# Kernel optimization log

Hardware: AMD Instinct MI355X
Metric: run time of the kernel (lower is better)

The kernel has to match this reference:

```python
import jax, jax.numpy as jnp
import numpy as np

VEC, HID, B, S = 1280, 128, 4, 256
EPS = 1e-5


def _ln(x):
    m = x.mean(-1, keepdims=True)
    v = ((x - m) ** 2).mean(-1, keepdims=True)
    return (x - m) / jnp.sqrt(v + EPS)


def _add_attn(q_in, kv_in, Wq, Wk, wv):
    # Additive (Bahdanau) attention: scores[b,i,j] = wv . tanh(q[b,i] + k[b,j])
    q = q_in @ Wq            # [B, Sq, H]
    k = kv_in @ Wk           # [B, Sk, H]
    feat = jnp.tanh(q[:, :, None, :] + k[:, None, :, :])   # [B, Sq, Sk, H]
    scores = jnp.einsum('bijh,h->bij', feat, wv)
    attn = jax.nn.softmax(scores, axis=-1)
    return jnp.einsum('bij,bjd->bid', attn, kv_in)          # values = kv_in


def _res_fc(x, W1, b1, W2, b2):
    return jnp.maximum(x @ W1 + b1, 0.0) @ W2 + b2 + x


def setup_inputs() -> dict:
    key = jax.random.key(0)
    ks = iter(jax.random.split(key, 64))
    d = {
        'X': jax.random.normal(next(ks), (B, S, VEC), dtype=jnp.float32),
        'lys_pos': 100,
    }
    sc = 0.02
    for i in (1, 2, 3, 4):
        d[f'Wq{i}'] = jax.random.normal(next(ks), (VEC, HID), dtype=jnp.float32) * sc
        d[f'Wk{i}'] = jax.random.normal(next(ks), (VEC, HID), dtype=jnp.float32) * sc
        d[f'wv{i}'] = jax.random.normal(next(ks), (HID,), dtype=jnp.float32) * sc
    for i in (1, 2, 3):
        d[f'rW1_{i}'] = jax.random.normal(next(ks), (VEC, HID), dtype=jnp.float32) * sc
        d[f'rb1_{i}'] = jnp.zeros((HID,), dtype=jnp.float32)
        d[f'rW2_{i}'] = jax.random.normal(next(ks), (HID, VEC), dtype=jnp.float32) * sc
        d[f'rb2_{i}'] = jnp.zeros((VEC,), dtype=jnp.float32)
    d['hW1'] = jax.random.normal(next(ks), (VEC, 32), dtype=jnp.float32) * sc
    d['hb1'] = jnp.zeros((32,), dtype=jnp.float32)
    d['hW2'] = jax.random.normal(next(ks), (32, 12), dtype=jnp.float32) * sc
    d['hb2'] = jnp.zeros((12,), dtype=jnp.float32)
    d['hW3'] = jax.random.normal(next(ks), (12, 2), dtype=jnp.float32) * sc
    d['hb3'] = jnp.zeros((2,), dtype=jnp.float32)
    return d


def reference(X, lys_pos,
              Wq1, Wk1, wv1, Wq2, Wk2, wv2, Wq3, Wk3, wv3, Wq4, Wk4, wv4,
              rW1_1, rb1_1, rW2_1, rb2_1,
              rW1_2, rb1_2, rW2_2, rb2_2,
              rW1_3, rb1_3, rW2_3, rb2_3,
              hW1, hb1, hW2, hb2, hW3, hb3):
    X = X.astype(jnp.float32)
    X = _ln(_add_attn(X, X, Wq1, Wk1, wv1) + X)
    X = _res_fc(X, rW1_1, rb1_1, rW2_1, rb2_1)
    X = _ln(_add_attn(X, X, Wq2, Wk2, wv2) + X)
    X = _res_fc(X, rW1_2, rb1_2, rW2_2, rb2_2)
    X = _ln(_add_attn(X, X, Wq3, Wk3, wv3) + X)
    X = _res_fc(X, rW1_3, rb1_3, rW2_3, rb2_3)
    X_lys = X[:, lys_pos, :][:, None, :]                    # [B, 1, VEC]
    X_lys = _ln(_add_attn(X_lys, X, Wq4, Wk4, wv4) + X_lys)
    h = jnp.maximum(X_lys @ hW1 + hb1, 0.0)                 # dropout = identity (eval)
    h = jnp.maximum(h @ hW2 + hb2, 0.0)
    logits = (h @ hW3 + hb3)[:, 0, :]                       # squeeze(1) -> [B, 2]
    return logits
```

## Files before the change

kernel.cpp:

```cpp
#include <hip/hip_runtime.h>


#define DEV __device__ __forceinline__

static constexpr int VEC = 1280;
static constexpr int HID = 128;
static constexpr int BB  = 4;
static constexpr int SS  = 256;
static constexpr int NPART = 8;
static constexpr long QK_PS = 262144;
static constexpr long H_PS  = 131072;
static constexpr int NBLK  = 512;
static constexpr int NSPLIT_NONE = 1 << 30;

typedef float f32x4 __attribute__((ext_vector_type(4)));

struct Params {
  const float* X; const int* lys;
  const float* Wq[4]; const float* Wk[4]; const float* wv[4];
  const float* rW1[3]; const float* rb1[3]; const float* rW2[3]; const float* rb2[3];
  const float* hW1; const float* hb1; const float* hW2; const float* hb2;
  const float* hW3; const float* hb3;
  float* QKp[4]; float* Qd[4]; float* KT[4];
  float* attn[3]; float* Yraw[3]; float* Yb[3];
  float* Hp[3]; float* Xout[3];
  float* out;
  unsigned* bar;
};

DEV void stcc(float* p, float v) {
  union { float f; unsigned u; } c; c.f = v;
  __hip_atomic_store((unsigned*)p, c.u, __ATOMIC_RELAXED,
                     __HIP_MEMORY_SCOPE_AGENT);
}
DEV void stcc4(float* p, float x, float y, float z, float w) {
  f32x4 v; v[0] = x; v[1] = y; v[2] = z; v[3] = w;
  asm volatile("global_store_dwordx4 %0, %1, off sc0 sc1"
               :: "v"(p), "v"(v) : "memory");
}

DEV float ftanh(float x) {
  float e = __expf(2.0f * x);
  return 1.0f - __fdividef(2.0f, e + 1.0f);
}

DEV float waveSum(float v) {
#pragma unroll
  for (int off = 32; off > 0; off >>= 1) v += __shfl_xor(v, off, 64);
  return v;
}
DEV float waveMax(float v) {
#pragma unroll
  for (int off = 32; off > 0; off >>= 1) v = fmaxf(v, __shfl_xor(v, off, 64));
  return v;
}
DEV float blockSum(float v, float* red) {
  v = waveSum(v);
  int tid = threadIdx.x;
  if ((tid & 63) == 0) red[tid >> 6] = v;
  __syncthreads();
  float r = (red[0] + red[1]) + (red[2] + red[3]);
  __syncthreads();
  return r;
}
DEV float blockMax(float v, float* red) {
  v = waveMax(v);
  int tid = threadIdx.x;
  if ((tid & 63) == 0) red[tid >> 6] = v;
  __syncthreads();
  float r = fmaxf(fmaxf(red[0], red[1]), fmaxf(red[2], red[3]));
  __syncthreads();
  return r;
}

DEV void gsync(unsigned* bar, unsigned target) {
  __syncthreads();
  if (threadIdx.x == 0) {
    asm volatile("s_waitcnt vmcnt(0)" ::: "memory");
    unsigned* grp  = bar + ((blockIdx.x >> 6) << 5);
    unsigned* root = bar + 256;
    unsigned* gen  = bar + 288;
    unsigned c = __hip_atomic_fetch_add(grp, 1u, __ATOMIC_RELAXED,
                                        __HIP_MEMORY_SCOPE_AGENT);
    if (c + 1u == target * 64u) {
      unsigned r = __hip_atomic_fetch_add(root, 1u, __ATOMIC_RELAXED,
                                          __HIP_MEMORY_SCOPE_AGENT);
      if (r + 1u == target * 8u) {
        __hip_atomic_store(gen, target, __ATOMIC_RELAXED,
                           __HIP_MEMORY_SCOPE_AGENT);
      }
    }
    while (__hip_atomic_load(gen, __ATOMIC_RELAXED,
                             __HIP_MEMORY_SCOPE_AGENT) < target)
      __builtin_amdgcn_s_sleep(2);
  }
  __syncthreads();
}

template <int MODE, bool AFUSE, bool OBIAS, bool ORES>
DEV void gemm_task(int n0, int m0, int z,
                   const float* __restrict__ A, long sAb, long aPart,
                   const float* __restrict__ B0, const float* __restrict__ B1,
                   int nSplitB, long sBb, int ldB,
                   float* __restrict__ C, long sCb,
                   const float* __restrict__ aBias,
                   const float* __restrict__ oBias,
                   const float* __restrict__ res,
                   int N, int K, int kChunk) {
  __shared__ float As[16][68];
  __shared__ float Bs[16][68];

  const float* Ab = A + (MODE == 2 ? (long)z * sAb : 0L);
  float*       Cb = C + (MODE >= 1 ? (long)z * sCb : 0L);
  const float* resz = ORES ? (res + (MODE == 2 ? (long)z * sCb : 0L)) : nullptr;
  const float* Bsel;
  int nb;
  if (n0 < nSplitB) { Bsel = B0; nb = n0; } else { Bsel = B1; nb = n0 - nSplitB; }
  if (MODE == 2) Bsel += (long)z * sBb;

  const int kBeg = (MODE == 1) ? z * kChunk : 0;
  const int kEnd = (MODE == 1) ? kBeg + kChunk : K;

  const int tid = threadIdx.x;
  const int tx = tid & 15, ty = tid >> 4;
  const int ar = tid >> 2, ac = (tid & 3) << 2;
  const int br = tid >> 4, bc = (tid & 15) << 2;

  auto loadA = [&](int kt) -> float4 {
    const size_t aoff = (size_t)(m0 + ar) * K + kt + ac;
    if (AFUSE) {
      float4 s = *(const float4*)(Ab + aoff);
#pragma unroll
      for (int p = 1; p < NPART; ++p) {
        const float4 t = *(const float4*)(Ab + (long)p * aPart + aoff);
        s.x += t.x; s.y += t.y; s.z += t.z; s.w += t.w;
      }
      const float4 bz = *(const float4*)(aBias + kt + ac);
      s.x = fmaxf(s.x + bz.x, 0.0f);
      s.y = fmaxf(s.y + bz.y, 0.0f);
      s.z = fmaxf(s.z + bz.z, 0.0f);
      s.w = fmaxf(s.w + bz.w, 0.0f);
      return s;
    }
    return *(const float4*)(Ab + aoff);
  };
  auto loadB = [&](int kt) -> float4 {
    return *(const float4*)(Bsel + (size_t)(kt + br) * ldB + nb + bc);
  };
  auto stAB = [&](const float4& a4, const float4& b4) {
    As[ac + 0][ar] = a4.x;
    As[ac + 1][ar] = a4.y;
    As[ac + 2][ar] = a4.z;
    As[ac + 3][ar] = a4.w;
    *(float4*)&Bs[br][bc] = b4;
  };

  float acc[4][4] = {};
  auto domath = [&]() {
#pragma unroll
    for (int kk = 0; kk < 16; ++kk) {
      const float4 av = *(const float4*)&As[kk][ty << 2];
      const float4 bv = *(const float4*)&Bs[kk][tx << 2];
      const float a[4] = {av.x, av.y, av.z, av.w};
      const float b[4] = {bv.x, bv.y, bv.z, bv.w};
#pragma unroll
      for (int i = 0; i < 4; ++i)
#pragma unroll
        for (int j = 0; j < 4; ++j) acc[i][j] = fmaf(a[i], b[j], acc[i][j]);
    }
  };

  if constexpr (!AFUSE) {
    float4 aA = loadA(kBeg), bA = loadB(kBeg);
    float4 aB = aA, bB = bA;
    if (kBeg + 16 < kEnd) { aB = loadA(kBeg + 16); bB = loadB(kBeg + 16); }
    for (int kt = kBeg; kt < kEnd; kt += 32) {
      __syncthreads();
      stAB(aA, bA);
      __syncthreads();
      if (kt + 32 < kEnd) { aA = loadA(kt + 32); bA = loadB(kt + 32); }
      domath();
      if (kt + 16 < kEnd) {
        __syncthreads();
        stAB(aB, bB);
        __syncthreads();
        if (kt + 48 < kEnd) { aB = loadA(kt + 48); bB = loadB(kt + 48); }
        domath();
      }
    }
  } else {
    float4 a4 = loadA(kBeg), b4 = loadB(kBeg);
    for (int kt = kBeg; kt < kEnd; kt += 16) {
      __syncthreads();
      stAB(a4, b4);
      __syncthreads();
      if (kt + 16 < kEnd) { a4 = loadA(kt + 16); b4 = loadB(kt + 16); }
      domath();
    }
  }

#pragma unroll
  for (int i = 0; i < 4; ++i) {
    const int m = m0 + (ty << 2) + i;
    const int n = n0 + (tx << 2);
    float o[4] = {acc[i][0], acc[i][1], acc[i][2], acc[i][3]};
    if (OBIAS) {
#pragma unroll
      for (int j = 0; j < 4; ++j) o[j] += oBias[n + j];
    }
    if (ORES) {
      const float4 r4 = *(const float4*)(resz + (size_t)m * N + n);
      o[0] += r4.x; o[1] += r4.y; o[2] += r4.z; o[3] += r4.w;
    }
    stcc4(&Cb[(size_t)m * N + n], o[0], o[1], o[2], o[3]);
  }
}

DEV void qksum_task(int r, const float* __restrict__ QKp,
                    float* __restrict__ Qd, float* __restrict__ KT) {
  const int tid = threadIdx.x;
  const int b = r >> 8, j = r & 255;
  const size_t off = (size_t)r * 256 + tid;
  float v = 0.0f;
#pragma unroll
  for (int p = 0; p < NPART; ++p) v += QKp[(long)p * QK_PS + off];
  if (tid < 128) {
    stcc(Qd + (size_t)r * 128 + tid, v);
  } else {
    stcc(KT + (size_t)b * 32768 + (size_t)(tid - 128) * 256 + j, v);
  }
}

DEV void scores_task(int t, const float* __restrict__ Qd,
                     const float* __restrict__ KT,
                     const float* __restrict__ wv,
                     float* __restrict__ attn) {
  const int b = t >> 7, i0 = (t & 127) << 1, tid = threadIdx.x;
  __shared__ float qs[2][128], wvs[128], red[4];
  {
    const int rr = tid >> 7, h = tid & 127;
    qs[rr][h] = Qd[(size_t)(b * 256 + i0 + rr) * 128 + h];
  }
  if (tid < 128) wvs[tid] = wv[tid];
  __syncthreads();

  const float* KTb = KT + (size_t)b * 32768 + tid;
  float s0 = 0.0f, s1 = 0.0f;
#pragma unroll 4
  for (int h = 0; h < 128; h += 4) {
    const float k0 = KTb[(h + 0) * 256];
    const float k1 = KTb[(h + 1) * 256];
    const float k2 = KTb[(h + 2) * 256];
    const float k3 = KTb[(h + 3) * 256];
    const float w0 = wvs[h], w1 = wvs[h + 1], w2 = wvs[h + 2], w3 = wvs[h + 3];
    s0 += w0 * ftanh(qs[0][h] + k0) + w1 * ftanh(qs[0][h + 1] + k1) +
          w2 * ftanh(qs[0][h + 2] + k2) + w3 * ftanh(qs[0][h + 3] + k3);
    s1 += w0 * ftanh(qs[1][h] + k0) + w1 * ftanh(qs[1][h + 1] + k1) +
          w2 * ftanh(qs[1][h + 2] + k2) + w3 * ftanh(qs[1][h + 3] + k3);
  }
  {
    const float mx = blockMax(s0, red);
    const float e = __expf(s0 - mx);
    const float tot = blockSum(e, red);
    stcc(attn + (size_t)(b * 256 + i0) * 256 + tid, e / tot);
  }
  {
    const float mx = blockMax(s1, red);
    const float e = __expf(s1 - mx);
    const float tot = blockSum(e, red);
    stcc(attn + (size_t)(b * 256 + i0 + 1) * 256 + tid, e / tot);
  }
}

DEV void ln_task(int r, const float* __restrict__ A, float* __restrict__ Y) {
  __shared__ float red[4];
  __shared__ float xbuf[1280];
  const int tid = threadIdx.x;
  const float* a = A + (size_t)r * VEC;
  float v[5];
  float sum = 0.0f;
#pragma unroll
  for (int k = 0; k < 5; ++k) {
    v[k] = a[tid + k * 256];
    sum += v[k];
  }
  sum = blockSum(sum, red);
  const float m = sum * (1.0f / VEC);
  float sq = 0.0f;
#pragma unroll
  for (int k = 0; k < 5; ++k) {
    const float dl = v[k] - m;
    sq += dl * dl;
  }
  sq = blockSum(sq, red);
  const float rstd = rsqrtf(sq * (1.0f / VEC) + 1e-5f);
#pragma unroll
  for (int k = 0; k < 5; ++k) xbuf[tid + k * 256] = (v[k] - m) * rstd;
  __syncthreads();
  float* y = Y + (size_t)r * VEC;
  {
    const float* x = xbuf + (tid << 2);
    stcc4(y + (tid << 2), x[0], x[1], x[2], x[3]);
  }
  if (tid < 64) {
    const float* x = xbuf + 1024 + (tid << 2);
    stcc4(y + 1024 + (tid << 2), x[0], x[1], x[2], x[3]);
  }
  __syncthreads();
}

DEV void tail_task(int b, const Params& p) {
  __shared__ float qs[128], wvs[128], red[4], aws[256];
  __shared__ float xrow[1280], partial[256];
  __shared__ float h1s[32], h2s[12];
  const int tid = threadIdx.x;
  const int lp = p.lys[0];
  const float* X3 = p.Xout[2];
  const float* Qd = p.Qd[3];
  const float* KT = p.KT[3];

  if (tid < 128) {
    qs[tid] = Qd[(size_t)(b * 256 + lp) * 128 + tid];
    wvs[tid] = p.wv[3][tid];
  }
  __syncthreads();
  const float* KTb = KT + (size_t)b * 32768 + tid;
  float s = 0.0f;
#pragma unroll 4
  for (int h = 0; h < 128; h += 4) {
    s += wvs[h + 0] * ftanh(qs[h + 0] + KTb[(h + 0) * 256]);
    s += wvs[h + 1] * ftanh(qs[h + 1] + KTb[(h + 1) * 256]);
    s += wvs[h + 2] * ftanh(qs[h + 2] + KTb[(h + 2) * 256]);
    s += wvs[h + 3] * ftanh(qs[h + 3] + KTb[(h + 3) * 256]);
  }
  const float mx = blockMax(s, red);
  const float e = __expf(s - mx);
  const float tot = blockSum(e, red);
  aws[tid] = e / tot;
  __syncthreads();

  const float* Xb = X3 + (size_t)b * SS * VEC;
  float v[5] = {};
#pragma unroll 2
  for (int j = 0; j < 256; ++j) {
    const float aw = aws[j];
    const float* xr = Xb + (size_t)j * VEC + tid;
#pragma unroll
    for (int k = 0; k < 5; ++k) v[k] = fmaf(aw, xr[k * 256], v[k]);
  }
#pragma unroll
  for (int k = 0; k < 5; ++k) v[k] += Xb[(size_t)lp * VEC + tid + k * 256];

  float sum = (v[0] + v[1]) + (v[2] + v[3]) + v[4];
  sum = blockSum(sum, red);
  const float m = sum * (1.0f / VEC);
  float sq = 0.0f;
#pragma unroll
  for (int k = 0; k < 5; ++k) {
    const float dl = v[k] - m;
    sq += dl * dl;
  }
  sq = blockSum(sq, red);
  const float rstd = rsqrtf(sq * (1.0f / VEC) + 1e-5f);
#pragma unroll
  for (int k = 0; k < 5; ++k) xrow[tid + k * 256] = (v[k] - m) * rstd;
  __syncthreads();

  {
    const int n = tid & 31, sl = tid >> 5;
    float pacc = 0.0f;
    for (int k = sl * 160; k < sl * 160 + 160; ++k)
      pacc = fmaf(xrow[k], p.hW1[(size_t)k * 32 + n], pacc);
    partial[tid] = pacc;
  }
  __syncthreads();
  if (tid < 32) {
    float t2 = 0.0f;
#pragma unroll
    for (int s2 = 0; s2 < 8; ++s2) t2 += partial[s2 * 32 + tid];
    h1s[tid] = fmaxf(t2 + p.hb1[tid], 0.0f);
  }
  __syncthreads();
  if (tid < 12) {
    float t2 = 0.0f;
#pragma unroll
    for (int k = 0; k < 32; ++k) t2 = fmaf(h1s[k], p.hW2[k * 12 + tid], t2);
    h2s[tid] = fmaxf(t2 + p.hb2[tid], 0.0f);
  }
  __syncthreads();
  if (tid < 2) {
    float t2 = 0.0f;
#pragma unroll
    for (int k = 0; k < 12; ++k) t2 = fmaf(h2s[k], p.hW3[k * 2 + tid], t2);
    p.out[b * 2 + tid] = t2 + p.hb3[tid];
  }
}

__global__ __launch_bounds__(256, 2) void mega_k(Params p) {
  const int bid = blockIdx.x;
  unsigned ph = 0;

  for (int l = 0; l < 4; ++l) {
    const float* Xin = (l == 0) ? p.X : p.Xout[l - 1];
    {
      const int x = bid & 3, y = (bid >> 2) & 15, z = bid >> 6;
      gemm_task<1, false, false, false>(x * 64, y * 64, z, Xin, 0L, 0L,
          p.Wq[l], p.Wk[l], HID, 0L, HID, p.QKp[l], QK_PS,
          nullptr, nullptr, nullptr, 2 * HID, VEC, 160);
    }
    gsync(p.bar, ++ph);
    qksum_task(bid, p.QKp[l], p.Qd[l], p.KT[l]);
    qksum_task(bid + NBLK, p.QKp[l], p.Qd[l], p.KT[l]);
    gsync(p.bar, ++ph);
    if (l == 3) break;
    scores_task(bid, p.Qd[l], p.KT[l], p.wv[l], p.attn[l]);
    gsync(p.bar, ++ph);
    if (bid < 320) {
      const int x = bid % 20, y = (bid / 20) & 3, zb = bid / 80;
      gemm_task<2, false, false, true>(x * 64, y * 64, zb, p.attn[l],
          (long)SS * SS, 0L, Xin, Xin, NSPLIT_NONE, (long)SS * VEC, VEC,
          p.Yraw[l], (long)SS * VEC, nullptr, nullptr, Xin, VEC, SS, 0);
    }
    gsync(p.bar, ++ph);
    ln_task(bid, p.Yraw[l], p.Yb[l]);
    ln_task(bid + NBLK, p.Yraw[l], p.Yb[l]);
    gsync(p.bar, ++ph);
    if (bid < 256) {
      const int x = bid & 1, y = (bid >> 1) & 15, z = bid >> 5;
      gemm_task<1, false, false, false>(x * 64, y * 64, z, p.Yb[l], 0L, 0L,
          p.rW1[l], p.rW1[l], NSPLIT_NONE, 0L, HID, p.Hp[l], H_PS,
          nullptr, nullptr, nullptr, HID, VEC, 160);
    }
    gsync(p.bar, ++ph);
    if (bid < 320) {
      const int x = bid % 20, y = bid / 20;
      gemm_task<0, true, true, true>(x * 64, y * 64, 0, p.Hp[l], 0L, H_PS,
          p.rW2[l], p.rW2[l], NSPLIT_NONE, 0L, VEC, p.Xout[l], 0L,
          p.rb1[l], p.rb2[l], p.Yb[l], VEC, HID, 0);
    }
    gsync(p.bar, ++ph);
  }
  if (bid < BB) tail_task(bid, p);
}

__global__ void initbar_k(unsigned* __restrict__ bar) {
  const int tid = threadIdx.x;
  for (int i = tid; i < 512; i += 256)
    __hip_atomic_store(bar + i, 0u, __ATOMIC_RELAXED,
                       __HIP_MEMORY_SCOPE_AGENT);
}

extern "C" void kernel_launch(void* const* d_in, const int* in_sizes, int n_in,
                              void* d_out, int out_size, void* d_ws, size_t ws_size,
                              hipStream_t stream) {
  Params p;
  p.X   = (const float*)d_in[0];
  p.lys = (const int*)d_in[1];
  p.Wq[0] = (const float*)d_in[2];  p.Wk[0] = (const float*)d_in[3];  p.wv[0] = (const float*)d_in[4];
  p.Wq[1] = (const float*)d_in[5];  p.Wk[1] = (const float*)d_in[6];  p.wv[1] = (const float*)d_in[7];
  p.Wq[2] = (const float*)d_in[8];  p.Wk[2] = (const float*)d_in[9];  p.wv[2] = (const float*)d_in[10];
  p.Wq[3] = (const float*)d_in[11]; p.Wk[3] = (const float*)d_in[12]; p.wv[3] = (const float*)d_in[13];
  p.rW1[0] = (const float*)d_in[14]; p.rb1[0] = (const float*)d_in[15];
  p.rW2[0] = (const float*)d_in[16]; p.rb2[0] = (const float*)d_in[17];
  p.rW1[1] = (const float*)d_in[18]; p.rb1[1] = (const float*)d_in[19];
  p.rW2[1] = (const float*)d_in[20]; p.rb2[1] = (const float*)d_in[21];
  p.rW1[2] = (const float*)d_in[22]; p.rb1[2] = (const float*)d_in[23];
  p.rW2[2] = (const float*)d_in[24]; p.rb2[2] = (const float*)d_in[25];
  p.hW1 = (const float*)d_in[26]; p.hb1 = (const float*)d_in[27];
  p.hW2 = (const float*)d_in[28]; p.hb2 = (const float*)d_in[29];
  p.hW3 = (const float*)d_in[30]; p.hb3 = (const float*)d_in[31];
  p.out = (float*)d_out;

  float* w = (float*)d_ws;
  for (int l = 0; l < 4; ++l) { p.QKp[l] = w; w += (long)NPART * QK_PS; }
  for (int l = 0; l < 4; ++l) { p.Qd[l]  = w; w += 131072; }
  for (int l = 0; l < 4; ++l) { p.KT[l]  = w; w += 131072; }
  for (int l = 0; l < 3; ++l) { p.attn[l] = w; w += 262144; }
  for (int l = 0; l < 3; ++l) { p.Yraw[l] = w; w += 1310720; }
  for (int l = 0; l < 3; ++l) { p.Yb[l]   = w; w += 1310720; }
  for (int l = 0; l < 3; ++l) { p.Hp[l]   = w; w += (long)NPART * H_PS; }
  for (int l = 0; l < 3; ++l) { p.Xout[l] = w; w += 1310720; }
  p.bar = (unsigned*)w;

  initbar_k<<<dim3(1), dim3(256), 0, stream>>>(p.bar);
  mega_k<<<dim3(NBLK), dim3(256), 0, stream>>>(p);
}
```

Before: 523.9 us.

## Fuse softmax, attention-value product and layernorm; retile FC GEMMs with dynamic tickets

The scores task now keeps the softmax weights in shared memory and directly computes the attention-weighted sum over X, adds the residual and applies layernorm. This removes the separate attn buffer, the AV GEMM, the Yraw buffer and two grid barriers per layer. The FC GEMMs switch to 32-row tiles so all blocks get work. The second FC GEMM pulls tiles from an atomic ticket counter, and the grid barrier's release flag is replicated per group to spread polling traffic. The fused AV loop reads the full X batch once for every pair of query rows, which may cost more memory traffic than the tiled GEMM it replaces.

```diff
diff --git a/kernel.cpp b/kernel.cpp
--- a/kernel.cpp
+++ b/kernel.cpp
@@ -22,8 +22,7 @@
   const float* hW1; const float* hb1; const float* hW2; const float* hb2;
   const float* hW3; const float* hb3;
   float* QKp[4]; float* Qd[4]; float* KT[4];
-  float* attn[3]; float* Yraw[3]; float* Yb[3];
-  float* Hp[3]; float* Xout[3];
+  float* Yb[3]; float* Hp[3]; float* Xout[3];
   float* out;
   unsigned* bar;
 };
@@ -77,19 +76,22 @@
   __syncthreads();
   if (threadIdx.x == 0) {
     asm volatile("s_waitcnt vmcnt(0)" ::: "memory");
-    unsigned* grp  = bar + ((blockIdx.x >> 6) << 5);
+    const int g = (int)(blockIdx.x >> 6);
+    unsigned* grp  = bar + (g << 5);
     unsigned* root = bar + 256;
-    unsigned* gen  = bar + 288;
     unsigned c = __hip_atomic_fetch_add(grp, 1u, __ATOMIC_RELAXED,
                                         __HIP_MEMORY_SCOPE_AGENT);
     if (c + 1u == target * 64u) {
       unsigned r = __hip_atomic_fetch_add(root, 1u, __ATOMIC_RELAXED,
                                           __HIP_MEMORY_SCOPE_AGENT);
       if (r + 1u == target * 8u) {
-        __hip_atomic_store(gen, target, __ATOMIC_RELAXED,
-                           __HIP_MEMORY_SCOPE_AGENT);
+#pragma unroll
+        for (int i = 0; i < 8; ++i)
+          __hip_atomic_store(bar + 288 + (i << 5), target, __ATOMIC_RELAXED,
+                             __HIP_MEMORY_SCOPE_AGENT);
       }
     }
+    unsigned* gen = bar + 288 + (g << 5);
     while (__hip_atomic_load(gen, __ATOMIC_RELAXED,
                              __HIP_MEMORY_SCOPE_AGENT) < target)
       __builtin_amdgcn_s_sleep(2);
@@ -97,111 +99,134 @@
   __syncthreads();
 }
 
-template <int MODE, bool AFUSE, bool OBIAS, bool ORES>
+template <int BM, int MODE, bool AFUSE, bool OBIAS, bool ORES>
 DEV void gemm_task(int n0, int m0, int z,
-                   const float* __restrict__ A, long sAb, long aPart,
+                   const float* __restrict__ A, long aPart,
                    const float* __restrict__ B0, const float* __restrict__ B1,
-                   int nSplitB, long sBb, int ldB,
+                   int nSplitB, int ldB,
                    float* __restrict__ C, long sCb,
                    const float* __restrict__ aBias,
                    const float* __restrict__ oBias,
                    const float* __restrict__ res,
                    int N, int K, int kChunk) {
-  __shared__ float As[16][68];
+  constexpr int MR = BM / 16;
+  constexpr int LDA = BM + 4;
+  __shared__ float As[16][LDA];
   __shared__ float Bs[16][68];
 
-  const float* Ab = A + (MODE == 2 ? (long)z * sAb : 0L);
-  float*       Cb = C + (MODE >= 1 ? (long)z * sCb : 0L);
-  const float* resz = ORES ? (res + (MODE == 2 ? (long)z * sCb : 0L)) : nullptr;
+  float* Cb = C + (MODE >= 1 ? (long)z * sCb : 0L);
   const float* Bsel;
   int nb;
   if (n0 < nSplitB) { Bsel = B0; nb = n0; } else { Bsel = B1; nb = n0 - nSplitB; }
-  if (MODE == 2) Bsel += (long)z * sBb;
 
   const int kBeg = (MODE == 1) ? z * kChunk : 0;
   const int kEnd = (MODE == 1) ? kBeg + kChunk : K;
 
   const int tid = threadIdx.x;
   const int tx = tid & 15, ty = tid >> 4;
-  const int ar = tid >> 2, ac = (tid & 3) << 2;
+  const int ar = tid / (16 / MR);
+  const int ac = (tid % (16 / MR)) * MR;
   const int br = tid >> 4, bc = (tid & 15) << 2;
 
-  auto loadA = [&](int kt) -> float4 {
+  struct FA { float v[MR]; };
+
+  auto loadA = [&](int kt) {
+    FA r;
+    const float* ap = A + (size_t)(m0 + ar) * K + kt + ac;
+    if constexpr (MR == 4) {
+      const float4 t = *(const float4*)ap;
+      r.v[0] = t.x; r.v[1] = t.y; r.v[2] = t.z; r.v[3] = t.w;
+    } else {
+      const float2 t = *(const float2*)ap;
+      r.v[0] = t.x; r.v[1] = t.y;
+    }
+    return r;
+  };
+  auto loadAF = [&](int kt) {
+    FA s;
+#pragma unroll
+    for (int q = 0; q < MR; ++q) s.v[q] = 0.0f;
     const size_t aoff = (size_t)(m0 + ar) * K + kt + ac;
-    if (AFUSE) {
-      float4 s = *(const float4*)(Ab + aoff);
-#pragma unroll
-      for (int p = 1; p < NPART; ++p) {
-        const float4 t = *(const float4*)(Ab + (long)p * aPart + aoff);
-        s.x += t.x; s.y += t.y; s.z += t.z; s.w += t.w;
+#pragma unroll
+    for (int p = 0; p < NPART; ++p) {
+      const float* ap = A + (long)p * aPart + aoff;
+      if constexpr (MR == 4) {
+        const float4 t = *(const float4*)ap;
+        s.v[0] += t.x; s.v[1] += t.y; s.v[2] += t.z; s.v[3] += t.w;
+      } else {
+        const float2 t = *(const float2*)ap;
+        s.v[0] += t.x; s.v[1] += t.y;
       }
-      const float4 bz = *(const float4*)(aBias + kt + ac);
-      s.x = fmaxf(s.x + bz.x, 0.0f);
-      s.y = fmaxf(s.y + bz.y, 0.0f);
-      s.z = fmaxf(s.z + bz.z, 0.0f);
-      s.w = fmaxf(s.w + bz.w, 0.0f);
-      return s;
-    }
-    return *(const float4*)(Ab + aoff);
+    }
+#pragma unroll
+    for (int q = 0; q < MR; ++q)
+      s.v[q] = fmaxf(s.v[q] + aBias[kt + ac + q], 0.0f);
+    return s;
   };
-  auto loadB = [&](int kt) -> float4 {
+  auto loadBf = [&](int kt) -> float4 {
     return *(const float4*)(Bsel + (size_t)(kt + br) * ldB + nb + bc);
   };
-  auto stAB = [&](const float4& a4, const float4& b4) {
-    As[ac + 0][ar] = a4.x;
-    As[ac + 1][ar] = a4.y;
-    As[ac + 2][ar] = a4.z;
-    As[ac + 3][ar] = a4.w;
-    *(float4*)&Bs[br][bc] = b4;
+  auto stAB = [&](const FA& a, const float4& b) {
+#pragma unroll
+    for (int q = 0; q < MR; ++q) As[ac + q][ar] = a.v[q];
+    *(float4*)&Bs[br][bc] = b;
   };
 
-  float acc[4][4] = {};
+  float acc[MR][4] = {};
   auto domath = [&]() {
 #pragma unroll
     for (int kk = 0; kk < 16; ++kk) {
-      const float4 av = *(const float4*)&As[kk][ty << 2];
-      const float4 bv = *(const float4*)&Bs[kk][tx << 2];
-      const float a[4] = {av.x, av.y, av.z, av.w};
-      const float b[4] = {bv.x, bv.y, bv.z, bv.w};
-#pragma unroll
-      for (int i = 0; i < 4; ++i)
+      float a[MR], b[4];
+      if constexpr (MR == 4) {
+        const float4 t = *(const float4*)&As[kk][ty << 2];
+        a[0] = t.x; a[1] = t.y; a[2] = t.z; a[3] = t.w;
+      } else {
+        const float2 t = *(const float2*)&As[kk][ty << 1];
+        a[0] = t.x; a[1] = t.y;
+      }
+      const float4 tb = *(const float4*)&Bs[kk][tx << 2];
+      b[0] = tb.x; b[1] = tb.y; b[2] = tb.z; b[3] = tb.w;
+#pragma unroll
+      for (int i = 0; i < MR; ++i)
 #pragma unroll
         for (int j = 0; j < 4; ++j) acc[i][j] = fmaf(a[i], b[j], acc[i][j]);
     }
   };
 
   if constexpr (!AFUSE) {
-    float4 aA = loadA(kBeg), bA = loadB(kBeg);
-    float4 aB = aA, bB = bA;
-    if (kBeg + 16 < kEnd) { aB = loadA(kBeg + 16); bB = loadB(kBeg + 16); }
+    FA aA = loadA(kBeg);
+    float4 bA = loadBf(kBeg);
+    FA aB = aA; float4 bB = bA;
+    if (kBeg + 16 < kEnd) { aB = loadA(kBeg + 16); bB = loadBf(kBeg + 16); }
     for (int kt = kBeg; kt < kEnd; kt += 32) {
       __syncthreads();
       stAB(aA, bA);
       __syncthreads();
-      if (kt + 32 < kEnd) { aA = loadA(kt + 32); bA = loadB(kt + 32); }
+      if (kt + 32 < kEnd) { aA = loadA(kt + 32); bA = loadBf(kt + 32); }
       domath();
       if (kt + 16 < kEnd) {
         __syncthreads();
         stAB(aB, bB);
         __syncthreads();
-        if (kt + 48 < kEnd) { aB = loadA(kt + 48); bB = loadB(kt + 48); }
+        if (kt + 48 < kEnd) { aB = loadA(kt + 48); bB = loadBf(kt + 48); }
         domath();
       }
     }
   } else {
-    float4 a4 = loadA(kBeg), b4 = loadB(kBeg);
+    FA a4 = loadAF(kBeg);
+    float4 b4 = loadBf(kBeg);
     for (int kt = kBeg; kt < kEnd; kt += 16) {
       __syncthreads();
       stAB(a4, b4);
       __syncthreads();
-      if (kt + 16 < kEnd) { a4 = loadA(kt + 16); b4 = loadB(kt + 16); }
+      if (kt + 16 < kEnd) { a4 = loadAF(kt + 16); b4 = loadBf(kt + 16); }
       domath();
     }
   }
 
 #pragma unroll
-  for (int i = 0; i < 4; ++i) {
-    const int m = m0 + (ty << 2) + i;
+  for (int i = 0; i < MR; ++i) {
+    const int m = m0 + ty * MR + i;
     const int n = n0 + (tx << 2);
     float o[4] = {acc[i][0], acc[i][1], acc[i][2], acc[i][3]};
     if (OBIAS) {
@@ -209,7 +234,7 @@
       for (int j = 0; j < 4; ++j) o[j] += oBias[n + j];
     }
     if (ORES) {
-      const float4 r4 = *(const float4*)(resz + (size_t)m * N + n);
+      const float4 r4 = *(const float4*)(res + (size_t)m * N + n);
       o[0] += r4.x; o[1] += r4.y; o[2] += r4.z; o[3] += r4.w;
     }
     stcc4(&Cb[(size_t)m * N + n], o[0], o[1], o[2], o[3]);
@@ -231,12 +256,13 @@
   }
 }
 
-DEV void scores_task(int t, const float* __restrict__ Qd,
-                     const float* __restrict__ KT,
-                     const float* __restrict__ wv,
-                     float* __restrict__ attn) {
+DEV void spl_task(int t, const float* __restrict__ Qd,
+                  const float* __restrict__ KT,
+                  const float* __restrict__ wv,
+                  const float* __restrict__ Xin,
+                  float* __restrict__ Yb) {
   const int b = t >> 7, i0 = (t & 127) << 1, tid = threadIdx.x;
-  __shared__ float qs[2][128], wvs[128], red[4];
+  __shared__ float qs[2][128], wvs[128], red[4], aws[2][256], xbuf[1280];
   {
     const int rr = tid >> 7, h = tid & 127;
     qs[rr][h] = Qd[(size_t)(b * 256 + i0 + rr) * 128 + h];
@@ -262,51 +288,64 @@
     const float mx = blockMax(s0, red);
     const float e = __expf(s0 - mx);
     const float tot = blockSum(e, red);
-    stcc(attn + (size_t)(b * 256 + i0) * 256 + tid, e / tot);
+    aws[0][tid] = e / tot;
   }
   {
     const float mx = blockMax(s1, red);
     const float e = __expf(s1 - mx);
     const float tot = blockSum(e, red);
-    stcc(attn + (size_t)(b * 256 + i0 + 1) * 256 + tid, e / tot);
-  }
-}
-
-DEV void ln_task(int r, const float* __restrict__ A, float* __restrict__ Y) {
-  __shared__ float red[4];
-  __shared__ float xbuf[1280];
-  const int tid = threadIdx.x;
-  const float* a = A + (size_t)r * VEC;
-  float v[5];
-  float sum = 0.0f;
-#pragma unroll
-  for (int k = 0; k < 5; ++k) {
-    v[k] = a[tid + k * 256];
-    sum += v[k];
-  }
-  sum = blockSum(sum, red);
-  const float m = sum * (1.0f / VEC);
-  float sq = 0.0f;
-#pragma unroll
-  for (int k = 0; k < 5; ++k) {
-    const float dl = v[k] - m;
-    sq += dl * dl;
-  }
-  sq = blockSum(sq, red);
-  const float rstd = rsqrtf(sq * (1.0f / VEC) + 1e-5f);
-#pragma unroll
-  for (int k = 0; k < 5; ++k) xbuf[tid + k * 256] = (v[k] - m) * rstd;
-  __syncthreads();
-  float* y = Y + (size_t)r * VEC;
-  {
-    const float* x = xbuf + (tid << 2);
-    stcc4(y + (tid << 2), x[0], x[1], x[2], x[3]);
-  }
-  if (tid < 64) {
-    const float* x = xbuf + 1024 + (tid << 2);
-    stcc4(y + 1024 + (tid << 2), x[0], x[1], x[2], x[3]);
-  }
-  __syncthreads();
+    aws[1][tid] = e / tot;
+  }
+  __syncthreads();
+
+  const float* Xb = Xin + (size_t)b * SS * VEC;
+  float a0[5] = {}, a1[5] = {};
+#pragma unroll 2
+  for (int j = 0; j < 256; ++j) {
+    const float w0 = aws[0][j], w1 = aws[1][j];
+    const float* xr = Xb + (size_t)j * VEC + tid;
+#pragma unroll
+    for (int k = 0; k < 5; ++k) {
+      const float x = xr[k * 256];
+      a0[k] = fmaf(w0, x, a0[k]);
+      a1[k] = fmaf(w1, x, a1[k]);
+    }
+  }
+
+#pragma unroll
+  for (int r = 0; r < 2; ++r) {
+    const float* xres = Xb + (size_t)(i0 + r) * VEC + tid;
+    float v[5];
+    float sum = 0.0f;
+#pragma unroll
+    for (int k = 0; k < 5; ++k) {
+      v[k] = (r ? a1[k] : a0[k]) + xres[k * 256];
+      sum += v[k];
+    }
+    sum = blockSum(sum, red);
+    const float m = sum * (1.0f / VEC);
+    float sq = 0.0f;
+#pragma unroll
+    for (int k = 0; k < 5; ++k) {
+      const float dl = v[k] - m;
+      sq += dl * dl;
+    }
+    sq = blockSum(sq, red);
+    const float rstd = rsqrtf(sq * (1.0f / VEC) + 1e-5f);
+#pragma unroll
+    for (int k = 0; k < 5; ++k) xbuf[tid + k * 256] = (v[k] - m) * rstd;
+    __syncthreads();
+    float* y = Yb + (size_t)(b * 256 + i0 + r) * VEC;
+    {
+      const float* x = xbuf + (tid << 2);
+      stcc4(y + (tid << 2), x[0], x[1], x[2], x[3]);
+    }
+    if (tid < 64) {
+      const float* x = xbuf + 1024 + (tid << 2);
+      stcc4(y + 1024 + (tid << 2), x[0], x[1], x[2], x[3]);
+    }
+    __syncthreads();
+  }
 }
 
 DEV void tail_task(int b, const Params& p) {
@@ -397,6 +436,7 @@
 }
 
 __global__ __launch_bounds__(256, 2) void mega_k(Params p) {
+  __shared__ int tkt;
   const int bid = blockIdx.x;
   unsigned ph = 0;
 
@@ -404,8 +444,8 @@
     const float* Xin = (l == 0) ? p.X : p.Xout[l - 1];
     {
       const int x = bid & 3, y = (bid >> 2) & 15, z = bid >> 6;
-      gemm_task<1, false, false, false>(x * 64, y * 64, z, Xin, 0L, 0L,
-          p.Wq[l], p.Wk[l], HID, 0L, HID, p.QKp[l], QK_PS,
+      gemm_task<64, 1, false, false, false>(x * 64, y * 64, z, Xin, 0L,
+          p.Wq[l], p.Wk[l], HID, HID, p.QKp[l], QK_PS,
           nullptr, nullptr, nullptr, 2 * HID, VEC, 160);
     }
     gsync(p.bar, ++ph);
@@ -413,30 +453,29 @@
     qksum_task(bid + NBLK, p.QKp[l], p.Qd[l], p.KT[l]);
     gsync(p.bar, ++ph);
     if (l == 3) break;
-    scores_task(bid, p.Qd[l], p.KT[l], p.wv[l], p.attn[l]);
+    spl_task(bid, p.Qd[l], p.KT[l], p.wv[l], Xin, p.Yb[l]);
     gsync(p.bar, ++ph);
-    if (bid < 320) {
-      const int x = bid % 20, y = (bid / 20) & 3, zb = bid / 80;
-      gemm_task<2, false, false, true>(x * 64, y * 64, zb, p.attn[l],
-          (long)SS * SS, 0L, Xin, Xin, NSPLIT_NONE, (long)SS * VEC, VEC,
-          p.Yraw[l], (long)SS * VEC, nullptr, nullptr, Xin, VEC, SS, 0);
+    {
+      const int x = bid & 1, y = (bid >> 1) & 31, z = bid >> 6;
+      gemm_task<32, 1, false, false, false>(x * 64, y * 32, z, p.Yb[l], 0L,
+          p.rW1[l], p.rW1[l], NSPLIT_NONE, HID, p.Hp[l], H_PS,
+          nullptr, nullptr, nullptr, HID, VEC, 160);
     }
     gsync(p.bar, ++ph);
-    ln_task(bid, p.Yraw[l], p.Yb[l]);
-    ln_task(bid + NBLK, p.Yraw[l], p.Yb[l]);
-    gsync(p.bar, ++ph);
-    if (bid < 256) {
-      const int x = bid & 1, y = (bid >> 1) & 15, z = bid >> 5;
-      gemm_task<1, false, false, false>(x * 64, y * 64, z, p.Yb[l], 0L, 0L,
-          p.rW1[l], p.rW1[l], NSPLIT_NONE, 0L, HID, p.Hp[l], H_PS,
-          nullptr, nullptr, nullptr, HID, VEC, 160);
-    }
-    gsync(p.bar, ++ph);
-    if (bid < 320) {
-      const int x = bid % 20, y = bid / 20;
-      gemm_task<0, true, true, true>(x * 64, y * 64, 0, p.Hp[l], 0L, H_PS,
-          p.rW2[l], p.rW2[l], NSPLIT_NONE, 0L, VEC, p.Xout[l], 0L,
-          p.rb1[l], p.rb2[l], p.Yb[l], VEC, HID, 0);
+    {
+      unsigned* tick = p.bar + 1024 + (l << 5);
+      for (;;) {
+        if (threadIdx.x == 0)
+          tkt = (int)__hip_atomic_fetch_add(tick, 1u, __ATOMIC_RELAXED,
+                                            __HIP_MEMORY_SCOPE_AGENT);
+        __syncthreads();
+        const int t = tkt;
+        if (t >= 640) break;
+        const int x = t % 20, y = t / 20;
+        gemm_task<32, 0, true, true, true>(x * 64, y * 32, 0, p.Hp[l], H_PS,
+            p.rW2[l], p.rW2[l], NSPLIT_NONE, VEC, p.Xout[l], 0L,
+            p.rb1[l], p.rb2[l], p.Yb[l], VEC, HID, 0);
+      }
     }
     gsync(p.bar, ++ph);
   }
@@ -445,7 +484,7 @@
 
 __global__ void initbar_k(unsigned* __restrict__ bar) {
   const int tid = threadIdx.x;
-  for (int i = tid; i < 512; i += 256)
+  for (int i = tid; i < 2048; i += 256)
     __hip_atomic_store(bar + i, 0u, __ATOMIC_RELAXED,
                        __HIP_MEMORY_SCOPE_AGENT);
 }
@@ -475,8 +514,6 @@
   for (int l = 0; l < 4; ++l) { p.QKp[l] = w; w += (long)NPART * QK_PS; }
   for (int l = 0; l < 4; ++l) { p.Qd[l]  = w; w += 131072; }
   for (int l = 0; l < 4; ++l) { p.KT[l]  = w; w += 131072; }
-  for (int l = 0; l < 3; ++l) { p.attn[l] = w; w += 262144; }
-  for (int l = 0; l < 3; ++l) { p.Yraw[l] = w; w += 1310720; }
   for (int l = 0; l < 3; ++l) { p.Yb[l]   = w; w += 1310720; }
   for (int l = 0; l < 3; ++l) { p.Hp[l]   = w; w += (long)NPART * H_PS; }
   for (int l = 0; l < 3; ++l) { p.Xout[l] = w; w += 1310720; }
```

New measurement: 636.3 us. 21.5% more time.

## Raise persistent grid to 768 blocks, share LDS arena, split hidden reduction phase

Applied to the files above, without the earlier changes.

The persistent megakernel grows from 512 to 768 blocks with launch bounds raised to four blocks per SM. The per-task shared arrays are merged into one shared arena so each block uses less LDS. The grid barrier now uses 12 groups, and the root writes a generation flag per group so waiters spin on separate lines. The second FC GEMM no longer sums the 8 hidden partials plus bias and ReLU inside its A-load. A separate hsum phase does that reduction once, which removes the repeated 8-way reduction at the cost of one extra grid barrier per layer. Most phases still run on at most 512 blocks, so the extra blocks mostly just join the barriers.

```diff
diff --git a/kernel.cpp b/kernel.cpp
--- a/kernel.cpp
+++ b/kernel.cpp
@@ -10,8 +10,10 @@
 static constexpr int NPART = 8;
 static constexpr long QK_PS = 262144;
 static constexpr long H_PS  = 131072;
-static constexpr int NBLK  = 512;
+static constexpr int NBLK  = 768;
+static constexpr int NGRP  = 12;
 static constexpr int NSPLIT_NONE = 1 << 30;
+static constexpr int ARENA_F = 2176;
 
 typedef float f32x4 __attribute__((ext_vector_type(4)));
 
@@ -23,7 +25,7 @@
   const float* hW3; const float* hb3;
   float* QKp[4]; float* Qd[4]; float* KT[4];
   float* attn[3]; float* Yraw[3]; float* Yb[3];
-  float* Hp[3]; float* Xout[3];
+  float* Hp[3]; float* Hd[3]; float* Xout[3];
   float* out;
   unsigned* bar;
 };
@@ -77,19 +79,22 @@
   __syncthreads();
   if (threadIdx.x == 0) {
     asm volatile("s_waitcnt vmcnt(0)" ::: "memory");
-    unsigned* grp  = bar + ((blockIdx.x >> 6) << 5);
-    unsigned* root = bar + 256;
-    unsigned* gen  = bar + 288;
+    const int g = (int)(blockIdx.x >> 6);
+    unsigned* grp  = bar + (g << 5);
+    unsigned* root = bar + 512;
     unsigned c = __hip_atomic_fetch_add(grp, 1u, __ATOMIC_RELAXED,
                                         __HIP_MEMORY_SCOPE_AGENT);
     if (c + 1u == target * 64u) {
       unsigned r = __hip_atomic_fetch_add(root, 1u, __ATOMIC_RELAXED,
                                           __HIP_MEMORY_SCOPE_AGENT);
-      if (r + 1u == target * 8u) {
-        __hip_atomic_store(gen, target, __ATOMIC_RELAXED,
-                           __HIP_MEMORY_SCOPE_AGENT);
+      if (r + 1u == target * (unsigned)NGRP) {
+#pragma unroll
+        for (int i = 0; i < NGRP; ++i)
+          __hip_atomic_store(bar + 544 + (i << 5), target, __ATOMIC_RELAXED,
+                             __HIP_MEMORY_SCOPE_AGENT);
       }
     }
+    unsigned* gen = bar + 544 + (g << 5);
     while (__hip_atomic_load(gen, __ATOMIC_RELAXED,
                              __HIP_MEMORY_SCOPE_AGENT) < target)
       __builtin_amdgcn_s_sleep(2);
@@ -97,18 +102,17 @@
   __syncthreads();
 }
 
-template <int MODE, bool AFUSE, bool OBIAS, bool ORES>
-DEV void gemm_task(int n0, int m0, int z,
-                   const float* __restrict__ A, long sAb, long aPart,
+template <int MODE, bool OBIAS, bool ORES>
+DEV void gemm_task(float* smem, int n0, int m0, int z,
+                   const float* __restrict__ A, long sAb,
                    const float* __restrict__ B0, const float* __restrict__ B1,
                    int nSplitB, long sBb, int ldB,
                    float* __restrict__ C, long sCb,
-                   const float* __restrict__ aBias,
                    const float* __restrict__ oBias,
                    const float* __restrict__ res,
                    int N, int K, int kChunk) {
-  __shared__ float As[16][68];
-  __shared__ float Bs[16][68];
+  float (*As)[68] = (float (*)[68])smem;
+  float (*Bs)[68] = (float (*)[68])(smem + 1088);
 
   const float* Ab = A + (MODE == 2 ? (long)z * sAb : 0L);
   float*       Cb = C + (MODE >= 1 ? (long)z * sCb : 0L);
@@ -127,22 +131,7 @@
   const int br = tid >> 4, bc = (tid & 15) << 2;
 
   auto loadA = [&](int kt) -> float4 {
-    const size_t aoff = (size_t)(m0 + ar) * K + kt + ac;
-    if (AFUSE) {
-      float4 s = *(const float4*)(Ab + aoff);
-#pragma unroll
-      for (int p = 1; p < NPART; ++p) {
-        const float4 t = *(const float4*)(Ab + (long)p * aPart + aoff);
-        s.x += t.x; s.y += t.y; s.z += t.z; s.w += t.w;
-      }
-      const float4 bz = *(const float4*)(aBias + kt + ac);
-      s.x = fmaxf(s.x + bz.x, 0.0f);
-      s.y = fmaxf(s.y + bz.y, 0.0f);
-      s.z = fmaxf(s.z + bz.z, 0.0f);
-      s.w = fmaxf(s.w + bz.w, 0.0f);
-      return s;
-    }
-    return *(const float4*)(Ab + aoff);
+    return *(const float4*)(Ab + (size_t)(m0 + ar) * K + kt + ac);
   };
   auto loadB = [&](int kt) -> float4 {
     return *(const float4*)(Bsel + (size_t)(kt + br) * ldB + nb + bc);
@@ -170,31 +159,20 @@
     }
   };
 
-  if constexpr (!AFUSE) {
-    float4 aA = loadA(kBeg), bA = loadB(kBeg);
-    float4 aB = aA, bB = bA;
-    if (kBeg + 16 < kEnd) { aB = loadA(kBeg + 16); bB = loadB(kBeg + 16); }
-    for (int kt = kBeg; kt < kEnd; kt += 32) {
+  float4 aA = loadA(kBeg), bA = loadB(kBeg);
+  float4 aB = aA, bB = bA;
+  if (kBeg + 16 < kEnd) { aB = loadA(kBeg + 16); bB = loadB(kBeg + 16); }
+  for (int kt = kBeg; kt < kEnd; kt += 32) {
+    __syncthreads();
+    stAB(aA, bA);
+    __syncthreads();
+    if (kt + 32 < kEnd) { aA = loadA(kt + 32); bA = loadB(kt + 32); }
+    domath();
+    if (kt + 16 < kEnd) {
       __syncthreads();
-      stAB(aA, bA);
+      stAB(aB, bB);
       __syncthreads();
-      if (kt + 32 < kEnd) { aA = loadA(kt + 32); bA = loadB(kt + 32); }
-      domath();
-      if (kt + 16 < kEnd) {
-        __syncthreads();
-        stAB(aB, bB);
-        __syncthreads();
-        if (kt + 48 < kEnd) { aB = loadA(kt + 48); bB = loadB(kt + 48); }
-        domath();
-      }
-    }
-  } else {
-    float4 a4 = loadA(kBeg), b4 = loadB(kBeg);
-    for (int kt = kBeg; kt < kEnd; kt += 16) {
-      __syncthreads();
-      stAB(a4, b4);
-      __syncthreads();
-      if (kt + 16 < kEnd) { a4 = loadA(kt + 16); b4 = loadB(kt + 16); }
+      if (kt + 48 < kEnd) { aB = loadA(kt + 48); bB = loadB(kt + 48); }
       domath();
     }
   }
@@ -231,12 +209,25 @@
   }
 }
 
-DEV void scores_task(int t, const float* __restrict__ Qd,
+DEV void hsum_task(int rp, const float* __restrict__ Hp,
+                   const float* __restrict__ b1, float* __restrict__ Hd) {
+  const int tid = threadIdx.x;
+  const int r = (rp << 1) | (tid >> 7), c = tid & 127;
+  const size_t off = (size_t)r * HID + c;
+  float v = 0.0f;
+#pragma unroll
+  for (int p = 0; p < NPART; ++p) v += Hp[(long)p * H_PS + off];
+  stcc(Hd + off, fmaxf(v + b1[c], 0.0f));
+}
+
+DEV void scores_task(float* smem, int t, const float* __restrict__ Qd,
                      const float* __restrict__ KT,
                      const float* __restrict__ wv,
                      float* __restrict__ attn) {
   const int b = t >> 7, i0 = (t & 127) << 1, tid = threadIdx.x;
-  __shared__ float qs[2][128], wvs[128], red[4];
+  float (*qs)[128] = (float (*)[128])smem;
+  float* wvs = smem + 256;
+  float* red = smem + 384;
   {
     const int rr = tid >> 7, h = tid & 127;
     qs[rr][h] = Qd[(size_t)(b * 256 + i0 + rr) * 128 + h];
@@ -272,9 +263,10 @@
   }
 }
 
-DEV void ln_task(int r, const float* __restrict__ A, float* __restrict__ Y) {
-  __shared__ float red[4];
-  __shared__ float xbuf[1280];
+DEV void ln_task(float* smem, int r, const float* __restrict__ A,
+                 float* __restrict__ Y) {
+  float* xbuf = smem;
+  float* red = smem + 1280;
   const int tid = threadIdx.x;
   const float* a = A + (size_t)r * VEC;
   float v[5];
@@ -309,10 +301,15 @@
   __syncthreads();
 }
 
-DEV void tail_task(int b, const Params& p) {
-  __shared__ float qs[128], wvs[128], red[4], aws[256];
-  __shared__ float xrow[1280], partial[256];
-  __shared__ float h1s[32], h2s[12];
+DEV void tail_task(float* smem, int b, const Params& p) {
+  float* qs = smem;
+  float* wvs = smem + 128;
+  float* red = smem + 256;
+  float* aws = smem + 260;
+  float* xrow = smem + 516;
+  float* partial = smem + 1796;
+  float* h1s = smem + 2052;
+  float* h2s = smem + 2084;
   const int tid = threadIdx.x;
   const int lp = p.lys[0];
   const float* X3 = p.Xout[2];
@@ -396,56 +393,59 @@
   }
 }
 
-__global__ __launch_bounds__(256, 2) void mega_k(Params p) {
+__global__ __launch_bounds__(256, 4) void mega_k(Params p) {
+  __shared__ float smem[ARENA_F];
   const int bid = blockIdx.x;
   unsigned ph = 0;
 
   for (int l = 0; l < 4; ++l) {
     const float* Xin = (l == 0) ? p.X : p.Xout[l - 1];
-    {
+    if (bid < 512) {
       const int x = bid & 3, y = (bid >> 2) & 15, z = bid >> 6;
-      gemm_task<1, false, false, false>(x * 64, y * 64, z, Xin, 0L, 0L,
+      gemm_task<1, false, false>(smem, x * 64, y * 64, z, Xin, 0L,
           p.Wq[l], p.Wk[l], HID, 0L, HID, p.QKp[l], QK_PS,
-          nullptr, nullptr, nullptr, 2 * HID, VEC, 160);
+          nullptr, nullptr, 2 * HID, VEC, 160);
     }
     gsync(p.bar, ++ph);
     qksum_task(bid, p.QKp[l], p.Qd[l], p.KT[l]);
-    qksum_task(bid + NBLK, p.QKp[l], p.Qd[l], p.KT[l]);
+    if (bid < 256) qksum_task(bid + NBLK, p.QKp[l], p.Qd[l], p.KT[l]);
     gsync(p.bar, ++ph);
     if (l == 3) break;
-    scores_task(bid, p.Qd[l], p.KT[l], p.wv[l], p.attn[l]);
+    if (bid < 512) scores_task(smem, bid, p.Qd[l], p.KT[l], p.wv[l], p.attn[l]);
     gsync(p.bar, ++ph);
     if (bid < 320) {
       const int x = bid % 20, y = (bid / 20) & 3, zb = bid / 80;
-      gemm_task<2, false, false, true>(x * 64, y * 64, zb, p.attn[l],
-          (long)SS * SS, 0L, Xin, Xin, NSPLIT_NONE, (long)SS * VEC, VEC,
-          p.Yraw[l], (long)SS * VEC, nullptr, nullptr, Xin, VEC, SS, 0);
-    }
-    gsync(p.bar, ++ph);
-    ln_task(bid, p.Yraw[l], p.Yb[l]);
-    ln_task(bid + NBLK, p.Yraw[l], p.Yb[l]);
+      gemm_task<2, false, true>(smem, x * 64, y * 64, zb, p.attn[l],
+          (long)SS * SS, Xin, Xin, NSPLIT_NONE, (long)SS * VEC, VEC,
+          p.Yraw[l], (long)SS * VEC, nullptr, Xin, VEC, SS, 0);
+    }
+    gsync(p.bar, ++ph);
+    ln_task(smem, bid, p.Yraw[l], p.Yb[l]);
+    if (bid < 256) ln_task(smem, bid + NBLK, p.Yraw[l], p.Yb[l]);
     gsync(p.bar, ++ph);
     if (bid < 256) {
       const int x = bid & 1, y = (bid >> 1) & 15, z = bid >> 5;
-      gemm_task<1, false, false, false>(x * 64, y * 64, z, p.Yb[l], 0L, 0L,
+      gemm_task<1, false, false>(smem, x * 64, y * 64, z, p.Yb[l], 0L,
           p.rW1[l], p.rW1[l], NSPLIT_NONE, 0L, HID, p.Hp[l], H_PS,
-          nullptr, nullptr, nullptr, HID, VEC, 160);
-    }
+          nullptr, nullptr, HID, VEC, 160);
+    }
+    gsync(p.bar, ++ph);
+    if (bid < 512) hsum_task(bid, p.Hp[l], p.rb1[l], p.Hd[l]);
     gsync(p.bar, ++ph);
     if (bid < 320) {
       const int x = bid % 20, y = bid / 20;
-      gemm_task<0, true, true, true>(x * 64, y * 64, 0, p.Hp[l], 0L, H_PS,
+      gemm_task<0, true, true>(smem, x * 64, y * 64, 0, p.Hd[l], 0L,
           p.rW2[l], p.rW2[l], NSPLIT_NONE, 0L, VEC, p.Xout[l], 0L,
-          p.rb1[l], p.rb2[l], p.Yb[l], VEC, HID, 0);
-    }
-    gsync(p.bar, ++ph);
-  }
-  if (bid < BB) tail_task(bid, p);
+          p.rb2[l], p.Yb[l], VEC, HID, 0);
+    }
+    gsync(p.bar, ++ph);
+  }
+  if (bid < BB) tail_task(smem, bid, p);
 }
 
 __global__ void initbar_k(unsigned* __restrict__ bar) {
   const int tid = threadIdx.x;
-  for (int i = tid; i < 512; i += 256)
+  for (int i = tid; i < 1024; i += 256)
     __hip_atomic_store(bar + i, 0u, __ATOMIC_RELAXED,
                        __HIP_MEMORY_SCOPE_AGENT);
 }
@@ -479,6 +479,7 @@
   for (int l = 0; l < 3; ++l) { p.Yraw[l] = w; w += 1310720; }
   for (int l = 0; l < 3; ++l) { p.Yb[l]   = w; w += 1310720; }
   for (int l = 0; l < 3; ++l) { p.Hp[l]   = w; w += (long)NPART * H_PS; }
+  for (int l = 0; l < 3; ++l) { p.Hd[l]   = w; w += 131072; }
   for (int l = 0; l < 3; ++l) { p.Xout[l] = w; w += 1310720; }
   p.bar = (unsigned*)w;
 
```

New measurement: 771.4 us. 1.47x slower.
